# Kernel tuning notes

Hardware: AMD Instinct MI355X
Metric: run time of the kernel (lower is better)

## Reference

```python
import jax, jax.numpy as jnp
import numpy as np

T, N_IN, R1, R2 = 1000, 4096, 4000, 4000
ALPHA1 = ALPHA2 = 0.5
GAMMA1 = GAMMA2 = 0.01
RHO1 = RHO2 = 1.0
SPARSITY = 0.9


def _sparse_reservoir(key, n, sparsity, rho):
    # Mirrors createSparseMatrix + spectral-radius normalization.
    k1, k2 = jax.random.split(key)
    W = jax.random.uniform(k1, (n, n), minval=-1.0, maxval=1.0, dtype=jnp.float32)
    mask = jax.random.uniform(k2, (n, n)) > sparsity
    W = W * mask
    # approximate spectral radius via power iteration
    def body(v, _):
        v = W @ v
        return v / jnp.linalg.norm(v), None
    v0 = jnp.ones((n,), jnp.float32) / jnp.sqrt(jnp.float32(n))
    v, _ = jax.lax.scan(body, v0, None, length=60)
    sr = jnp.linalg.norm(W @ v)
    return rho * W / sr


def setup_inputs() -> dict:
    key = jax.random.key(0)
    kx, kw1, kw2, kr1, kr2 = jax.random.split(key, 5)
    x = jax.random.normal(kx, (T, N_IN), dtype=jnp.float32)
    Win1 = GAMMA1 * jax.random.normal(kw1, (N_IN, R1), dtype=jnp.float32)
    Win2 = GAMMA2 * jax.random.normal(kw2, (R1, R2), dtype=jnp.float32)
    W1 = _sparse_reservoir(kr1, R1, SPARSITY, RHO1)
    W2 = _sparse_reservoir(kr2, R2, SPARSITY, RHO2)
    return {"x": x, "Win1": Win1, "W1": W1, "Win2": Win2, "W2": W2}


def reference(x, Win1, W1, Win2, W2):
    # Hierarchical leaky-integrator ESN: rows of x are consecutive timesteps.
    a1, a2 = ALPHA1, ALPHA2

    def step(carry, u):
        v1, v2 = carry  # [R1], [R2]
        v1n = (1.0 - a1) * v1 + a1 * jnp.tanh(v1 @ W1 + u @ Win1)
        v2n = (1.0 - a2) * v2 + a2 * jnp.tanh(v2 @ W2 + v1n @ Win2)
        return (v1n, v2n), jnp.concatenate([v1n, v2n])

    init = (jnp.zeros((W1.shape[0],), x.dtype), jnp.zeros((W2.shape[0],), x.dtype))
    _, out = jax.lax.scan(step, init, x)  # out: [T, R1+R2]
    return out
```

## Files before the change

kernel.cpp:

```cpp
#include <hip/hip_runtime.h>
#include <hip/hip_bf16.h>


typedef __bf16 bf16;
typedef __bf16 bf16x8 __attribute__((ext_vector_type(8)));
typedef float  f32x4  __attribute__((ext_vector_type(4)));
typedef unsigned uint4v __attribute__((ext_vector_type(4)));

#define RDIM 4000
#define TSTEPS 1000
#define CAP 640
#define NBLK 250
#define CB 16
#define CH 8

__device__ inline unsigned pack_rne(float w, unsigned row) {
    unsigned u = __float_as_uint(w);
    return ((u + 0x7FFFu + ((u >> 16) & 1u)) & 0xFFFF0000u) | row;
}

__global__ __launch_bounds__(256) void count_k(const float* __restrict__ W,
                                               unsigned* __restrict__ cnts) {
    int j = blockIdx.x * 256 + threadIdx.x;
    int c = blockIdx.y;
    if (j >= RDIM) return;
    unsigned n = 0;
    const float* p = W + (size_t)c * 500 * RDIM + j;
    for (int i = 0; i < 500; i++) n += (p[(size_t)i * RDIM] != 0.0f);
    cnts[c * RDIM + j] = n;
}

__global__ __launch_bounds__(256) void offs_k(unsigned* __restrict__ cnts,
                                              unsigned* __restrict__ offs) {
    int j = blockIdx.x * 256 + threadIdx.x;
    if (j >= RDIM) return;
    unsigned run = 0;
    for (int c = 0; c < CH; c++) {
        offs[c * RDIM + j] = run;
        run += cnts[c * RDIM + j];
    }
    cnts[j] = run;
}

__global__ __launch_bounds__(256) void kmax_k(const unsigned* __restrict__ totals,
                                              int* __restrict__ kmax) {
    int b = blockIdx.x * 256 + threadIdx.x;
    if (b >= NBLK) return;
    unsigned m = 0;
    for (int jl = 0; jl < CB; jl++) {
        unsigned t = totals[b * CB + jl];
        m = t > m ? t : m;
    }
    m = (m + 3) >> 2;
    kmax[b] = (int)(m < (CAP / 4) ? m : (CAP / 4));
}

__global__ __launch_bounds__(256) void fill_k(const float* __restrict__ W,
                                              const unsigned* __restrict__ offs,
                                              unsigned* __restrict__ P) {
    int j = blockIdx.x * 256 + threadIdx.x;
    int c = blockIdx.y;
    if (j >= RDIM) return;
    unsigned slot = offs[c * RDIM + j];
    unsigned base = (unsigned)(j >> 4) * (CAP * CB) + (unsigned)(j & 15) * 4;
    int r0 = c * 500;
    for (int i = 0; i < 500; i++) {
        float w = W[(size_t)(r0 + i) * RDIM + j];
        if (w != 0.0f) {
            if (slot < CAP)
                P[base + (slot >> 2) * (CB * 4) + (slot & 3)] =
                    pack_rne(w, (unsigned)(r0 + i));
            slot++;
        }
    }
}

#define BM 64
#define BN 64
#define BK 32
#define LDP 56

__device__ inline bf16x8 load8(const float* p) {
    const f32x4* q = (const f32x4*)p;
    f32x4 f0 = q[0], f1 = q[1];
    bf16x8 r;
    r[0] = (bf16)f0[0]; r[1] = (bf16)f0[1]; r[2] = (bf16)f0[2]; r[3] = (bf16)f0[3];
    r[4] = (bf16)f1[0]; r[5] = (bf16)f1[1]; r[6] = (bf16)f1[2]; r[7] = (bf16)f1[3];
    return r;
}
__device__ inline bf16x8 load8(const bf16* p) { return *(const bf16x8*)p; }

template <typename AT>
__global__ __launch_bounds__(256) void gemm_k(const AT* __restrict__ A,
                                              const float* __restrict__ B,
                                              float* __restrict__ C,
                                              int M, int N, int K,
                                              int lda, int ldb, int ldc) {
    __shared__ bf16 As[BM][LDP];
    __shared__ bf16 Bs[BN][LDP];
    int tid  = threadIdx.x;
    int wave = tid >> 6, lane = tid & 63;
    int q    = lane >> 4;
    int l16  = lane & 15;
    int m0 = blockIdx.y * BM;
    int n0 = blockIdx.x * BN;

    int arow = tid >> 2;
    int acol = (tid & 3) * 8;
    int brow = tid >> 3;
    int bcol = (tid & 7) * 8;

    f32x4 acc[4];
    for (int nb = 0; nb < 4; nb++) for (int r = 0; r < 4; r++) acc[nb][r] = 0.f;

    for (int k0 = 0; k0 < K; k0 += BK) {
        bf16x8 av; for (int e = 0; e < 8; e++) av[e] = (bf16)0.f;
        if (m0 + arow < M)
            av = load8(A + (size_t)(m0 + arow) * lda + k0 + acol);
        bf16x8 bv;
        if (n0 + bcol + 8 <= N)
            bv = load8(B + (size_t)(k0 + brow) * ldb + n0 + bcol);
        else {
            for (int e = 0; e < 8; e++) {
                int col = n0 + bcol + e;
                bv[e] = (col < N) ? (bf16)B[(size_t)(k0 + brow) * ldb + col] : (bf16)0.f;
            }
        }
        __syncthreads();
        *(bf16x8*)&As[arow][acol] = av;
        for (int e = 0; e < 8; e++) Bs[bcol + e][brow] = bv[e];
        __syncthreads();

        bf16x8 af = *(const bf16x8*)&As[wave * 16 + l16][q * 8];
        #pragma unroll
        for (int nb = 0; nb < 4; nb++) {
            bf16x8 bfr = *(const bf16x8*)&Bs[nb * 16 + l16][q * 8];
            acc[nb] = __builtin_amdgcn_mfma_f32_16x16x32_bf16(af, bfr, acc[nb], 0, 0, 0);
        }
    }
    for (int nb = 0; nb < 4; nb++)
        for (int r = 0; r < 4; r++) {
            int row = m0 + wave * 16 + q * 4 + r;
            int col = n0 + nb * 16 + l16;
            if (row < M && col < N) C[(size_t)row * ldc + col] = acc[nb][r];
        }
}

__global__ __launch_bounds__(512, 2) void scan_coop(
        const unsigned* __restrict__ P, const int* __restrict__ kmax,
        const float* __restrict__ U, float* __restrict__ va, float* __restrict__ vb,
        float* __restrict__ outbase, bf16* __restrict__ vhist,
        unsigned* __restrict__ cnt) {
    __shared__ __align__(16) float vsh[RDIM];
    __shared__ float red[8 * CB];
    int tid = threadIdx.x, b = blockIdx.x;
    int jl = tid & (CB - 1), ks = tid >> 4;
    const unsigned* Pb = P + (size_t)b * (CAP * CB);
    int kg = kmax[b];

    for (int t = 0; t < TSTEPS; t++) {
        const float* vo = (t & 1) ? vb : va;
        float*       vn = (t & 1) ? va : vb;

        if (t > 0) {
            if (tid == 0) {
                unsigned target = (unsigned)NBLK * (unsigned)t;
                for (;;) {
                    unsigned s = 0;
                    #pragma unroll
                    for (int i = 0; i < 8; i++)
                        s += __hip_atomic_load(cnt + i * 8, __ATOMIC_RELAXED,
                                               __HIP_MEMORY_SCOPE_AGENT);
                    if (s >= target) break;
                    __builtin_amdgcn_s_sleep(1);
                }
            }
            __syncthreads();
        }

        float uval = 0.f;
        if (tid < CB) uval = U[(size_t)t * RDIM + b * CB + tid];

        float rv[8];
        #pragma unroll
        for (int u = 0; u < 8; u++) {
            int i = (u << 9) + tid;
            int ic = i < RDIM ? i : (RDIM - 1);
            rv[u] = __hip_atomic_load(vo + ic, __ATOMIC_RELAXED,
                                      __HIP_MEMORY_SCOPE_AGENT);
        }
        #pragma unroll
        for (int u = 0; u < 8; u++) {
            int i = (u << 9) + tid;
            if (i < RDIM) vsh[i] = rv[u];
        }
        __syncthreads();

        float acc = 0.f;
        for (int sg = ks; sg < kg; sg += 32) {
            uint4v p = *(const uint4v*)(Pb + sg * (CB * 4) + jl * 4);
            #pragma unroll
            for (int e = 0; e < 4; e++) {
                unsigned pe = p[e];
                acc += vsh[pe & 0xFFFFu] * __uint_as_float(pe & 0xFFFF0000u);
            }
        }
        acc += __shfl_xor(acc, 16, 64);
        acc += __shfl_xor(acc, 32, 64);
        int lane = tid & 63;
        if (lane < CB) red[(tid >> 6) * CB + lane] = acc;
        __syncthreads();
        if (tid < CB) {
            float s = 0.f;
            #pragma unroll
            for (int c = 0; c < 8; c++) s += red[c * CB + tid];
            int j = b * CB + tid;
            float vnj = 0.5f * vsh[j] + 0.5f * tanhf(s + uval);
            __hip_atomic_store(vn + j, vnj, __ATOMIC_RELAXED,
                               __HIP_MEMORY_SCOPE_AGENT);
            outbase[(size_t)t * 8000 + j] = vnj;
            if (vhist) vhist[(size_t)t * RDIM + j] = (bf16)vnj;
        }
        __syncthreads();
        if (tid == 0)
            __hip_atomic_fetch_add(cnt + (b & 7) * 8, 1u, __ATOMIC_RELAXED,
                                   __HIP_MEMORY_SCOPE_AGENT);
    }
}

extern "C" void kernel_launch(void* const* d_in, const int* in_sizes, int n_in,
                              void* d_out, int out_size, void* d_ws, size_t ws_size,
                              hipStream_t stream) {
    const float* x    = (const float*)d_in[0];
    const float* Win1 = (const float*)d_in[1];
    const float* W1   = (const float*)d_in[2];
    const float* Win2 = (const float*)d_in[3];
    const float* W2   = (const float*)d_in[4];
    float* out = (float*)d_out;

    char* ws = (char*)d_ws;
    float*    U     = (float*)(ws);
    unsigned* cnts  = (unsigned*)(ws);
    unsigned* offs  = (unsigned*)(ws + 128000);
    unsigned* P1    = (unsigned*)(ws + 16000000);
    unsigned* P2    = (unsigned*)(ws + 26240000);
    bf16*     V1bf  = (bf16*)(ws + 36480000);
    int*      kmax1 = (int*)(ws + 44480000);
    int*      kmax2 = (int*)(ws + 44482000);
    float*    vbuf  = (float*)(ws + 44484000);
    unsigned* cnt1  = (unsigned*)(ws + 44548000);
    unsigned* cnt2  = (unsigned*)(ws + 44548256);

    hipMemsetAsync(vbuf, 0, 4 * RDIM * sizeof(float), stream);
    hipMemsetAsync(cnt1, 0, 512, stream);
    hipMemsetAsync(P1, 0, (size_t)NBLK * CAP * CB * 4, stream);
    hipMemsetAsync(P2, 0, (size_t)NBLK * CAP * CB * 4, stream);

    dim3 cg16(16, CH);
    count_k<<<cg16, 256, 0, stream>>>(W1, cnts);
    offs_k<<<16, 256, 0, stream>>>(cnts, offs);
    kmax_k<<<1, 256, 0, stream>>>(cnts, kmax1);
    fill_k<<<cg16, 256, 0, stream>>>(W1, offs, P1);
    count_k<<<cg16, 256, 0, stream>>>(W2, cnts);
    offs_k<<<16, 256, 0, stream>>>(cnts, offs);
    kmax_k<<<1, 256, 0, stream>>>(cnts, kmax2);
    fill_k<<<cg16, 256, 0, stream>>>(W2, offs, P2);

    dim3 gg((RDIM + BN - 1) / BN, (TSTEPS + BM - 1) / BM);
    gemm_k<float><<<gg, 256, 0, stream>>>(x, Win1, U, TSTEPS, RDIM, 4096,
                                          4096, RDIM, RDIM);

    {
        const unsigned* Pp = P1; const int* km = kmax1; const float* Up = U;
        float* va = vbuf; float* vb = vbuf + RDIM;
        float* ob = out; bf16* vh = V1bf; unsigned* cn = cnt1;
        void* args[] = {&Pp, &km, &Up, &va, &vb, &ob, &vh, &cn};
        hipLaunchCooperativeKernel((void*)scan_coop, dim3(NBLK), dim3(512),
                                   args, 0, stream);
    }

    gemm_k<bf16><<<gg, 256, 0, stream>>>(V1bf, Win2, U, TSTEPS, RDIM, RDIM,
                                         RDIM, RDIM, RDIM);

    {
        const unsigned* Pp = P2; const int* km = kmax2; const float* Up = U;
        float* va = vbuf + 2 * RDIM; float* vb = vbuf + 3 * RDIM;
        float* ob = out + RDIM; bf16* vh = nullptr; unsigned* cn = cnt2;
        void* args[] = {&Pp, &km, &Up, &va, &vb, &ob, &vh, &cn};
        hipLaunchCooperativeKernel((void*)scan_coop, dim3(NBLK), dim3(512),
                                   args, 0, stream);
    }
}
```

Baseline: 7.652 ms.

## Streamline per-step grid sync: vector coherent loads, earlier signal, padded counters

Replaces the eight scalar atomic loads of the previous state vector with two 16-byte cache-bypassing global loads per thread (inline asm with sc0 sc1). Signals the step counter right after the new state values are stored and waited on, dropping the trailing block barrier and moving the output and history writes after the signal. Spreads the eight counters 64 bytes apart instead of 32, and replaces tanhf with an exp-based formula. The goal is to shorten the latency of each of the 1000 grid-synchronised steps. It relies on vmcnt ordering rather than a release fence, and the exp form may lose accuracy or overflow for large inputs.

After: 8.340 ms. +9.0%, slower.

```diff
diff --git a/kernel.cpp b/kernel.cpp
--- a/kernel.cpp
+++ b/kernel.cpp
@@ -17,6 +17,17 @@
 __device__ inline unsigned pack_rne(float w, unsigned row) {
     unsigned u = __float_as_uint(w);
     return ((u + 0x7FFFu + ((u >> 16) & 1u)) & 0xFFFF0000u) | row;
+}
+
+__device__ inline void stage2(const float* p0, const float* p1,
+                              f32x4& a, f32x4& b) {
+    asm volatile(
+        "global_load_dwordx4 %0, %2, off sc0 sc1\n\t"
+        "global_load_dwordx4 %1, %3, off sc0 sc1\n\t"
+        "s_waitcnt vmcnt(0)"
+        : "=&v"(a), "=&v"(b)
+        : "v"(p0), "v"(p1)
+        : "memory");
 }
 
 __global__ __launch_bounds__(256) void count_k(const float* __restrict__ W,
@@ -169,7 +180,7 @@
                     unsigned s = 0;
                     #pragma unroll
                     for (int i = 0; i < 8; i++)
-                        s += __hip_atomic_load(cnt + i * 8, __ATOMIC_RELAXED,
+                        s += __hip_atomic_load(cnt + i * 16, __ATOMIC_RELAXED,
                                                __HIP_MEMORY_SCOPE_AGENT);
                     if (s >= target) break;
                     __builtin_amdgcn_s_sleep(1);
@@ -181,18 +192,13 @@
         float uval = 0.f;
         if (tid < CB) uval = U[(size_t)t * RDIM + b * CB + tid];
 
-        float rv[8];
-        #pragma unroll
-        for (int u = 0; u < 8; u++) {
-            int i = (u << 9) + tid;
-            int ic = i < RDIM ? i : (RDIM - 1);
-            rv[u] = __hip_atomic_load(vo + ic, __ATOMIC_RELAXED,
-                                      __HIP_MEMORY_SCOPE_AGENT);
-        }
-        #pragma unroll
-        for (int u = 0; u < 8; u++) {
-            int i = (u << 9) + tid;
-            if (i < RDIM) vsh[i] = rv[u];
+        {
+            const f32x4* vo4 = (const f32x4*)vo;
+            int c1 = tid + 512; if (c1 > 999) c1 = 999;
+            f32x4 ra, rb;
+            stage2((const float*)(vo4 + tid), (const float*)(vo4 + c1), ra, rb);
+            ((f32x4*)vsh)[tid] = ra;
+            if (tid < 488) ((f32x4*)vsh)[tid + 512] = rb;
         }
         __syncthreads();
 
@@ -210,21 +216,27 @@
         int lane = tid & 63;
         if (lane < CB) red[(tid >> 6) * CB + lane] = acc;
         __syncthreads();
+
+        float vnj = 0.f;
+        int j = b * CB + (tid & (CB - 1));
         if (tid < CB) {
             float s = 0.f;
             #pragma unroll
             for (int c = 0; c < 8; c++) s += red[c * CB + tid];
-            int j = b * CB + tid;
-            float vnj = 0.5f * vsh[j] + 0.5f * tanhf(s + uval);
+            float z = s + uval;
+            float e2 = __expf(2.0f * z);
+            vnj = 0.5f * vsh[j] + 0.5f * (1.0f - 2.0f / (e2 + 1.0f));
             __hip_atomic_store(vn + j, vnj, __ATOMIC_RELAXED,
                                __HIP_MEMORY_SCOPE_AGENT);
+        }
+        asm volatile("s_waitcnt vmcnt(0)" ::: "memory");
+        if (tid == 0)
+            __hip_atomic_fetch_add(cnt + (b & 7) * 16, 1u, __ATOMIC_RELAXED,
+                                   __HIP_MEMORY_SCOPE_AGENT);
+        if (tid < CB) {
             outbase[(size_t)t * 8000 + j] = vnj;
             if (vhist) vhist[(size_t)t * RDIM + j] = (bf16)vnj;
         }
-        __syncthreads();
-        if (tid == 0)
-            __hip_atomic_fetch_add(cnt + (b & 7) * 8, 1u, __ATOMIC_RELAXED,
-                                   __HIP_MEMORY_SCOPE_AGENT);
     }
 }
 
@@ -248,11 +260,11 @@
     int*      kmax1 = (int*)(ws + 44480000);
     int*      kmax2 = (int*)(ws + 44482000);
     float*    vbuf  = (float*)(ws + 44484000);
-    unsigned* cnt1  = (unsigned*)(ws + 44548000);
-    unsigned* cnt2  = (unsigned*)(ws + 44548256);
+    unsigned* cnt1  = (unsigned*)(ws + 44548096);
+    unsigned* cnt2  = (unsigned*)(ws + 44548608);
 
     hipMemsetAsync(vbuf, 0, 4 * RDIM * sizeof(float), stream);
-    hipMemsetAsync(cnt1, 0, 512, stream);
+    hipMemsetAsync(cnt1, 0, 1024, stream);
     hipMemsetAsync(P1, 0, (size_t)NBLK * CAP * CB * 4, stream);
     hipMemsetAsync(P2, 0, (size_t)NBLK * CAP * CB * 4, stream);
 
```
